# Optimization experiments

Hardware: AMD Instinct MI355X
Metric: run time of the kernel (lower is better)

The kernel has to match this reference:

```python
import jax, jax.numpy as jnp
import numpy as np

C = 19
IGNORE = 255
UPPER_BOUND = 1.0
SEG_W, EDGE_W, ATT_W = 1.0, 0.3, 0.1
EDGE_THRESH = 0.8


def _img_hist(t):
    # torch.histc(target, bins=C, min=0, max=C): bin i counts values in [i, i+1); 255 falls outside
    tf = t.ravel()
    inb = (tf >= 0) & (tf < C)
    idx = jnp.where(inb, tf, 0)
    return jnp.zeros((C,), jnp.float32).at[idx].add(inb.astype(jnp.float32))


def _seg_loss(segin, target):
    # per-image class-histogram weights (ImageBasedCrossEntropyLoss2d, norm=False)
    N = target.shape[0]
    bins = jax.vmap(_img_hist)(target)                      # [N, C]
    hist_norm = bins / jnp.sum(bins, axis=1, keepdims=True)
    w = (bins != 0).astype(jnp.float32) * UPPER_BOUND * (1.0 - hist_norm) + 1.0  # [N, C]

    logp = jax.nn.log_softmax(segin, axis=1)                # [N, C, H, W]
    tc = jnp.clip(target, 0, C - 1)
    lp = jnp.take_along_axis(logp, tc[:, None, :, :], axis=1)[:, 0]  # [N, H, W]
    valid = (target != IGNORE).astype(jnp.float32)
    pw = jnp.take_along_axis(w, tc.reshape(N, -1), axis=1).reshape(target.shape) * valid
    # NLLLoss(weight, reduction='mean', ignore_index): weighted mean per image, summed over batch
    num = -jnp.sum(pw * lp, axis=(1, 2))
    den = jnp.sum(pw, axis=(1, 2))
    return jnp.sum(num / den)


def _bce2d(x, t):
    # x: logits [N,1,H,W]; t: float target, 1=pos, 0=neg, >1 ignored (weight 0)
    pos = t == 1.0
    neg = t == 0.0
    pos_num = jnp.sum(pos.astype(jnp.float32))
    neg_num = jnp.sum(neg.astype(jnp.float32))
    sum_num = pos_num + neg_num
    w = jnp.where(pos, neg_num / sum_num, 0.0) + jnp.where(neg, pos_num / sum_num, 0.0)
    # stable BCE-with-logits
    bce = jnp.maximum(x, 0.0) - x * t + jnp.log1p(jnp.exp(-jnp.abs(x)))
    return jnp.mean(w * bce)


def setup_inputs() -> dict:
    key = jax.random.key(0)
    k1, k2, k3, k4 = jax.random.split(key, 4)
    N, H, W = 4, 768, 768
    segin = jax.random.normal(k1, (N, C, H, W), dtype=jnp.float32)
    edgein = jax.random.normal(k2, (N, 1, H, W), dtype=jnp.float32)
    segmask = jax.random.randint(k3, (N, H, W), 0, C, dtype=jnp.int32)
    edgemask = jax.random.randint(k4, (N, 1, H, W), 0, 2, dtype=jnp.int32)
    return {"segin": segin, "edgein": edgein, "segmask": segmask, "edgemask": edgemask}


def reference(segin, edgein, segmask, edgemask):
    seg_loss = SEG_W * _seg_loss(segin, segmask)
    edge_loss = EDGE_W * _bce2d(edgein, edgemask.astype(jnp.float32))
    # edge attention: pixels where max-channel edge logit > 0.8 keep their label, else ignore
    edge_max = jnp.max(edgein, axis=1)                      # [N, H, W]
    att_target = jnp.where(edge_max > EDGE_THRESH, segmask, IGNORE)
    att_loss = ATT_W * _seg_loss(segin, att_target)
    return seg_loss + edge_loss + att_loss
```

## Files before the change

kernel.cpp:

```cpp
#include <hip/hip_runtime.h>
#include <math.h>

#define CNUM 19
#define NB 4
#define HW 589824
#define NPIX 2359296

struct Ws {
  unsigned int hist_seg[NB][CNUM];
  unsigned int hist_att[NB][CNUM];
  unsigned int pos_num;
  unsigned int neg_num;
  float w_seg[NB][CNUM];
  float w_att[NB][CNUM];
  double num_seg[NB];
  double den_seg[NB];
  double num_att[NB];
  double den_att[NB];
  double bce_sum;
};

__global__ void k_init(Ws* ws) {
  unsigned int* p = (unsigned int*)ws;
  const int nwords = (int)(sizeof(Ws) / 4);
  for (int i = threadIdx.x; i < nwords; i += blockDim.x) p[i] = 0u;
}

__global__ __launch_bounds__(256) void k_hist(const int* __restrict__ segmask,
                                              const float* __restrict__ edgein,
                                              const int* __restrict__ edgemask,
                                              Ws* __restrict__ ws) {
  const int n  = blockIdx.y;
  const int bx = blockIdx.x;
  const int tid = threadIdx.x;
  const int base = n * HW + bx * 4096 + tid * 4;

  unsigned int cs[CNUM], ca[CNUM];
  #pragma unroll
  for (int c = 0; c < CNUM; ++c) { cs[c] = 0u; ca[c] = 0u; }
  unsigned int cp = 0u, cn = 0u;

  #pragma unroll
  for (int it = 0; it < 4; ++it) {
    const int idx = base + it * 1024;
    int4   sv = *reinterpret_cast<const int4*>(segmask + idx);
    float4 e  = *reinterpret_cast<const float4*>(edgein + idx);
    int4   mv = *reinterpret_cast<const int4*>(edgemask + idx);
    int   sa[4] = {sv.x, sv.y, sv.z, sv.w};
    float ea[4] = {e.x, e.y, e.z, e.w};
    int   ma[4] = {mv.x, mv.y, mv.z, mv.w};
    #pragma unroll
    for (int p = 0; p < 4; ++p) {
      const int s = sa[p];
      const bool inb = ((unsigned)s) < (unsigned)CNUM;
      const bool att = inb && (ea[p] > 0.8f);
      #pragma unroll
      for (int c = 0; c < CNUM; ++c) {
        cs[c] += (unsigned)__popcll(__ballot(inb && (s == c)));
        ca[c] += (unsigned)__popcll(__ballot(att && (s == c)));
      }
      cp += (unsigned)__popcll(__ballot(ma[p] == 1));
      cn += (unsigned)__popcll(__ballot(ma[p] == 0));
    }
  }

  __shared__ unsigned int red[4][2 * CNUM + 2];
  const int wave = tid >> 6;
  const int lane = tid & 63;
  if (lane == 0) {
    #pragma unroll
    for (int c = 0; c < CNUM; ++c) { red[wave][c] = cs[c]; red[wave][CNUM + c] = ca[c]; }
    red[wave][2 * CNUM] = cp;
    red[wave][2 * CNUM + 1] = cn;
  }
  __syncthreads();
  if (tid < 2 * CNUM + 2) {
    unsigned int v = red[0][tid] + red[1][tid] + red[2][tid] + red[3][tid];
    if (tid < CNUM)               atomicAdd(&ws->hist_seg[n][tid], v);
    else if (tid < 2 * CNUM)      atomicAdd(&ws->hist_att[n][tid - CNUM], v);
    else if (tid == 2 * CNUM)     atomicAdd(&ws->pos_num, v);
    else                          atomicAdd(&ws->neg_num, v);
  }
}

__global__ void k_weights(Ws* ws) {
  int t = threadIdx.x;
  if (t < 2 * NB * CNUM) {
    int which = t / (NB * CNUM);
    int r = t % (NB * CNUM);
    int n = r / CNUM, c = r % CNUM;
    const unsigned int* h = which ? ws->hist_att[n] : ws->hist_seg[n];
    float total = 0.f;
    #pragma unroll
    for (int i = 0; i < CNUM; ++i) total += (float)h[i];
    float bins = (float)h[c];
    float w = (bins != 0.f ? (1.0f - bins / total) : 0.f) + 1.0f;
    if (which) ws->w_att[n][c] = w;
    else       ws->w_seg[n][c] = w;
  }
}

__global__ __launch_bounds__(256) void k_main(const float* __restrict__ segin,
                                              const float* __restrict__ edgein,
                                              const int* __restrict__ segmask,
                                              const int* __restrict__ edgemask,
                                              const Ws* __restrict__ ws,
                                              Ws* __restrict__ wsw) {
  const int n = blockIdx.y;
  const int tid = threadIdx.x;
  const int hw4 = (blockIdx.x * 256 + tid) * 4;
  const int idx4 = n * HW + hw4;
  const float* base = segin + (size_t)n * CNUM * HW + hw4;

  __shared__ float lws[CNUM], lwa[CNUM];
  if (tid < CNUM) lws[tid] = ws->w_seg[n][tid];
  else if (tid >= 64 && tid < 64 + CNUM) lwa[tid - 64] = ws->w_att[n][tid - 64];
  __syncthreads();

  int4   tm = *reinterpret_cast<const int4*>(segmask + idx4);
  float4 ev = *reinterpret_cast<const float4*>(edgein + idx4);
  int4   em = *reinterpret_cast<const int4*>(edgemask + idx4);
  int   tarr[4]  = {tm.x, tm.y, tm.z, tm.w};
  float earr[4]  = {ev.x, ev.y, ev.z, ev.w};
  int   emarr[4] = {em.x, em.y, em.z, em.w};

  int tc[4];
  #pragma unroll
  for (int p = 0; p < 4; ++p) tc[p] = min(max(tarr[p], 0), CNUM - 1);

  float s[4]  = {0.f, 0.f, 0.f, 0.f};
  float xt[4] = {0.f, 0.f, 0.f, 0.f};
  #pragma unroll
  for (int c = 0; c < CNUM; ++c) {
    float4 v = *reinterpret_cast<const float4*>(base + (size_t)c * HW);
    float va[4] = {v.x, v.y, v.z, v.w};
    #pragma unroll
    for (int p = 0; p < 4; ++p) {
      s[p] += __expf(va[p]);
      xt[p] = (tc[p] == c) ? va[p] : xt[p];
    }
  }

  const unsigned int pn = ws->pos_num, nn = ws->neg_num;
  const float inv_sum = 1.0f / (float)(pn + nn);
  const float wpos = (float)nn * inv_sum;
  const float wneg = (float)pn * inv_sum;

  float acc_num_s = 0.f, acc_den_s = 0.f, acc_num_a = 0.f, acc_den_a = 0.f, acc_bce = 0.f;
  #pragma unroll
  for (int p = 0; p < 4; ++p) {
    float lp = xt[p] - __logf(s[p]);
    bool validt = (tarr[p] != 255);
    float pw_s = validt ? lws[tc[p]] : 0.f;
    acc_num_s -= pw_s * lp;
    acc_den_s += pw_s;

    float e = earr[p];
    bool valida = validt && (e > 0.8f);
    float pw_a = valida ? lwa[tc[p]] : 0.f;
    acc_num_a -= pw_a * lp;
    acc_den_a += pw_a;

    int emv = emarr[p];
    float tf = (float)emv;
    float wb = (emv == 1) ? wpos : ((emv == 0) ? wneg : 0.f);
    float bce = fmaxf(e, 0.f) - e * tf + log1pf(__expf(-fabsf(e)));
    acc_bce += wb * bce;
  }

  #pragma unroll
  for (int off = 32; off > 0; off >>= 1) {
    acc_num_s += __shfl_down(acc_num_s, off);
    acc_den_s += __shfl_down(acc_den_s, off);
    acc_num_a += __shfl_down(acc_num_a, off);
    acc_den_a += __shfl_down(acc_den_a, off);
    acc_bce   += __shfl_down(acc_bce, off);
  }
  __shared__ float red[4][5];
  const int wave = tid >> 6;
  const int lane = tid & 63;
  if (lane == 0) {
    red[wave][0] = acc_num_s; red[wave][1] = acc_den_s;
    red[wave][2] = acc_num_a; red[wave][3] = acc_den_a;
    red[wave][4] = acc_bce;
  }
  __syncthreads();
  if (tid == 0) {
    float r0 = 0.f, r1 = 0.f, r2 = 0.f, r3 = 0.f, r4 = 0.f;
    #pragma unroll
    for (int wv = 0; wv < 4; ++wv) {
      r0 += red[wv][0]; r1 += red[wv][1]; r2 += red[wv][2];
      r3 += red[wv][3]; r4 += red[wv][4];
    }
    atomicAdd(&wsw->num_seg[n], (double)r0);
    atomicAdd(&wsw->den_seg[n], (double)r1);
    atomicAdd(&wsw->num_att[n], (double)r2);
    atomicAdd(&wsw->den_att[n], (double)r3);
    atomicAdd(&wsw->bce_sum,    (double)r4);
  }
}

__global__ void k_final(const Ws* __restrict__ ws, float* __restrict__ out) {
  if (threadIdx.x == 0 && blockIdx.x == 0) {
    double segl = 0.0, attl = 0.0;
    for (int i = 0; i < NB; ++i) {
      segl += ws->num_seg[i] / ws->den_seg[i];
      attl += ws->num_att[i] / ws->den_att[i];
    }
    double edgel = ws->bce_sum / (double)NPIX;
    out[0] = (float)(1.0 * segl + 0.3 * edgel + 0.1 * attl);
  }
}

extern "C" void kernel_launch(void* const* d_in, const int* in_sizes, int n_in,
                              void* d_out, int out_size, void* d_ws, size_t ws_size,
                              hipStream_t stream) {
  const float* segin   = (const float*)d_in[0];
  const float* edgein  = (const float*)d_in[1];
  const int*   segmask = (const int*)d_in[2];
  const int*   edgemask= (const int*)d_in[3];
  Ws* ws = (Ws*)d_ws;
  float* out = (float*)d_out;

  hipLaunchKernelGGL(k_init,    dim3(1),              dim3(256), 0, stream, ws);
  hipLaunchKernelGGL(k_hist,    dim3(HW / 4096, NB),  dim3(256), 0, stream, segmask, edgein, edgemask, ws);
  hipLaunchKernelGGL(k_weights, dim3(1),              dim3(256), 0, stream, ws);
  hipLaunchKernelGGL(k_main,    dim3(HW / 1024, NB),  dim3(256), 0, stream, segin, edgein, segmask, edgemask, ws, ws);
  hipLaunchKernelGGL(k_final,   dim3(1),              dim3(1),   0, stream, ws, out);
}
```

Measured before the change: 355.8 us.

## Fuse weight computation into main kernel and batch-load all channel logits

Removes the separate weights kernel: each main-kernel block now recomputes the per-image class weights from the histograms in shared memory. The main kernel issues all 19 channel float4 loads up front, before the barrier, to expose more memory-level parallelism, and sets launch bounds to cap register use. The histogram kernel reuses a single class ballot ANDed with an attention-mask ballot instead of issuing a second ballot per class. Holding 76 floats per thread raises register pressure, which the occupancy hint may turn into spills.

```diff
diff --git a/kernel.cpp b/kernel.cpp
--- a/kernel.cpp
+++ b/kernel.cpp
@@ -11,8 +11,6 @@
   unsigned int hist_att[NB][CNUM];
   unsigned int pos_num;
   unsigned int neg_num;
-  float w_seg[NB][CNUM];
-  float w_att[NB][CNUM];
   double num_seg[NB];
   double den_seg[NB];
   double num_att[NB];
@@ -53,11 +51,12 @@
     for (int p = 0; p < 4; ++p) {
       const int s = sa[p];
       const bool inb = ((unsigned)s) < (unsigned)CNUM;
-      const bool att = inb && (ea[p] > 0.8f);
+      const unsigned long long attm = __ballot(ea[p] > 0.8f);
       #pragma unroll
       for (int c = 0; c < CNUM; ++c) {
-        cs[c] += (unsigned)__popcll(__ballot(inb && (s == c)));
-        ca[c] += (unsigned)__popcll(__ballot(att && (s == c)));
+        unsigned long long bm = __ballot(inb && (s == c));
+        cs[c] += (unsigned)__popcll(bm);
+        ca[c] += (unsigned)__popcll(bm & attm);
       }
       cp += (unsigned)__popcll(__ballot(ma[p] == 1));
       cn += (unsigned)__popcll(__ballot(ma[p] == 0));
@@ -83,29 +82,12 @@
   }
 }
 
-__global__ void k_weights(Ws* ws) {
-  int t = threadIdx.x;
-  if (t < 2 * NB * CNUM) {
-    int which = t / (NB * CNUM);
-    int r = t % (NB * CNUM);
-    int n = r / CNUM, c = r % CNUM;
-    const unsigned int* h = which ? ws->hist_att[n] : ws->hist_seg[n];
-    float total = 0.f;
-    #pragma unroll
-    for (int i = 0; i < CNUM; ++i) total += (float)h[i];
-    float bins = (float)h[c];
-    float w = (bins != 0.f ? (1.0f - bins / total) : 0.f) + 1.0f;
-    if (which) ws->w_att[n][c] = w;
-    else       ws->w_seg[n][c] = w;
-  }
-}
-
-__global__ __launch_bounds__(256) void k_main(const float* __restrict__ segin,
-                                              const float* __restrict__ edgein,
-                                              const int* __restrict__ segmask,
-                                              const int* __restrict__ edgemask,
-                                              const Ws* __restrict__ ws,
-                                              Ws* __restrict__ wsw) {
+__global__ __launch_bounds__(256, 4) void k_main(const float* __restrict__ segin,
+                                                 const float* __restrict__ edgein,
+                                                 const int* __restrict__ segmask,
+                                                 const int* __restrict__ edgemask,
+                                                 const Ws* __restrict__ ws,
+                                                 Ws* __restrict__ wsw) {
   const int n = blockIdx.y;
   const int tid = threadIdx.x;
   const int hw4 = (blockIdx.x * 256 + tid) * 4;
@@ -113,51 +95,63 @@
   const float* base = segin + (size_t)n * CNUM * HW + hw4;
 
   __shared__ float lws[CNUM], lwa[CNUM];
-  if (tid < CNUM) lws[tid] = ws->w_seg[n][tid];
-  else if (tid >= 64 && tid < 64 + CNUM) lwa[tid - 64] = ws->w_att[n][tid - 64];
-  __syncthreads();
-
+  if (tid < CNUM) {
+    float total = 0.f;
+    #pragma unroll
+    for (int i = 0; i < CNUM; ++i) total += (float)ws->hist_seg[n][i];
+    float bins = (float)ws->hist_seg[n][tid];
+    lws[tid] = (bins != 0.f ? (1.0f - bins / total) : 0.f) + 1.0f;
+  } else if (tid >= 64 && tid < 64 + CNUM) {
+    int c = tid - 64;
+    float total = 0.f;
+    #pragma unroll
+    for (int i = 0; i < CNUM; ++i) total += (float)ws->hist_att[n][i];
+    float bins = (float)ws->hist_att[n][c];
+    lwa[c] = (bins != 0.f ? (1.0f - bins / total) : 0.f) + 1.0f;
+  }
+
+  float4 xv[CNUM];
+  #pragma unroll
+  for (int c = 0; c < CNUM; ++c)
+    xv[c] = *reinterpret_cast<const float4*>(base + (size_t)c * HW);
   int4   tm = *reinterpret_cast<const int4*>(segmask + idx4);
   float4 ev = *reinterpret_cast<const float4*>(edgein + idx4);
   int4   em = *reinterpret_cast<const int4*>(edgemask + idx4);
-  int   tarr[4]  = {tm.x, tm.y, tm.z, tm.w};
-  float earr[4]  = {ev.x, ev.y, ev.z, ev.w};
-  int   emarr[4] = {em.x, em.y, em.z, em.w};
-
-  int tc[4];
-  #pragma unroll
-  for (int p = 0; p < 4; ++p) tc[p] = min(max(tarr[p], 0), CNUM - 1);
-
-  float s[4]  = {0.f, 0.f, 0.f, 0.f};
-  float xt[4] = {0.f, 0.f, 0.f, 0.f};
-  #pragma unroll
-  for (int c = 0; c < CNUM; ++c) {
-    float4 v = *reinterpret_cast<const float4*>(base + (size_t)c * HW);
-    float va[4] = {v.x, v.y, v.z, v.w};
-    #pragma unroll
-    for (int p = 0; p < 4; ++p) {
-      s[p] += __expf(va[p]);
-      xt[p] = (tc[p] == c) ? va[p] : xt[p];
-    }
-  }
 
   const unsigned int pn = ws->pos_num, nn = ws->neg_num;
   const float inv_sum = 1.0f / (float)(pn + nn);
   const float wpos = (float)nn * inv_sum;
   const float wneg = (float)pn * inv_sum;
 
+  __syncthreads();
+
+  int   tarr[4]  = {tm.x, tm.y, tm.z, tm.w};
+  float earr[4]  = {ev.x, ev.y, ev.z, ev.w};
+  int   emarr[4] = {em.x, em.y, em.z, em.w};
+
   float acc_num_s = 0.f, acc_den_s = 0.f, acc_num_a = 0.f, acc_den_a = 0.f, acc_bce = 0.f;
   #pragma unroll
   for (int p = 0; p < 4; ++p) {
-    float lp = xt[p] - __logf(s[p]);
-    bool validt = (tarr[p] != 255);
-    float pw_s = validt ? lws[tc[p]] : 0.f;
+    const int t = tarr[p];
+    const int tc = min(max(t, 0), CNUM - 1);
+    const float* xp = (const float*)&xv[0] + p;
+    float s = 0.f, xt = 0.f;
+    #pragma unroll
+    for (int c = 0; c < CNUM; ++c) {
+      float v = xp[4 * c];
+      s += __expf(v);
+      xt = (tc == c) ? v : xt;
+    }
+    float lp = xt - __logf(s);
+
+    bool validt = (t != 255);
+    float pw_s = validt ? lws[tc] : 0.f;
     acc_num_s -= pw_s * lp;
     acc_den_s += pw_s;
 
     float e = earr[p];
     bool valida = validt && (e > 0.8f);
-    float pw_a = valida ? lwa[tc[p]] : 0.f;
+    float pw_a = valida ? lwa[tc] : 0.f;
     acc_num_a -= pw_a * lp;
     acc_den_a += pw_a;
 
@@ -222,9 +216,8 @@
   Ws* ws = (Ws*)d_ws;
   float* out = (float*)d_out;
 
-  hipLaunchKernelGGL(k_init,    dim3(1),              dim3(256), 0, stream, ws);
-  hipLaunchKernelGGL(k_hist,    dim3(HW / 4096, NB),  dim3(256), 0, stream, segmask, edgein, edgemask, ws);
-  hipLaunchKernelGGL(k_weights, dim3(1),              dim3(256), 0, stream, ws);
-  hipLaunchKernelGGL(k_main,    dim3(HW / 1024, NB),  dim3(256), 0, stream, segin, edgein, segmask, edgemask, ws, ws);
-  hipLaunchKernelGGL(k_final,   dim3(1),              dim3(1),   0, stream, ws, out);
-}
+  hipLaunchKernelGGL(k_init,  dim3(1),             dim3(256), 0, stream, ws);
+  hipLaunchKernelGGL(k_hist,  dim3(HW / 4096, NB), dim3(256), 0, stream, segmask, edgein, edgemask, ws);
+  hipLaunchKernelGGL(k_main,  dim3(HW / 1024, NB), dim3(256), 0, stream, segin, edgein, segmask, edgemask, ws, ws);
+  hipLaunchKernelGGL(k_final, dim3(1),             dim3(1),   0, stream, ws, out);
+}
```

Measured after the change: 345.8 us. 1.03x faster.

## Fold class weights algebraically to single-pass kernel with per-class partial sums

Applied to the files above, without the earlier changes.

Removes the separate histogram and weight kernels by accumulating, per image and class, the count and the sum of -log p. The final kernel then applies the histogram weights algebraically, and does the same for BCE by splitting positive and negative sums. The main kernel also stages segin tiles into LDS through global_load_lds and accumulates per-class sums with shared-memory atomics. This drops a full pass over the masks and two launches, at the cost of contended LDS float atomics and a large LDS footprint that lowers occupancy.

```diff
diff --git a/kernel.cpp b/kernel.cpp
--- a/kernel.cpp
+++ b/kernel.cpp
@@ -5,125 +5,63 @@
 #define NB 4
 #define HW 589824
 #define NPIX 2359296
+#define TILE 1024
 
 struct Ws {
-  unsigned int hist_seg[NB][CNUM];
-  unsigned int hist_att[NB][CNUM];
+  float S_seg[NB][CNUM];
+  float C_seg[NB][CNUM];
+  float S_att[NB][CNUM];
+  float C_att[NB][CNUM];
+  float B_pos;
+  float B_neg;
   unsigned int pos_num;
   unsigned int neg_num;
-  float w_seg[NB][CNUM];
-  float w_att[NB][CNUM];
-  double num_seg[NB];
-  double den_seg[NB];
-  double num_att[NB];
-  double den_att[NB];
-  double bce_sum;
 };
 
 __global__ void k_init(Ws* ws) {
   unsigned int* p = (unsigned int*)ws;
-  const int nwords = (int)(sizeof(Ws) / 4);
-  for (int i = threadIdx.x; i < nwords; i += blockDim.x) p[i] = 0u;
+  const int nw = (int)(sizeof(Ws) / 4);
+  for (int i = threadIdx.x; i < nw; i += blockDim.x) p[i] = 0u;
 }
 
-__global__ __launch_bounds__(256) void k_hist(const int* __restrict__ segmask,
-                                              const float* __restrict__ edgein,
-                                              const int* __restrict__ edgemask,
-                                              Ws* __restrict__ ws) {
-  const int n  = blockIdx.y;
-  const int bx = blockIdx.x;
+__global__ __launch_bounds__(256, 2) void k_main(const float* __restrict__ segin,
+                                                 const float* __restrict__ edgein,
+                                                 const int* __restrict__ segmask,
+                                                 const int* __restrict__ edgemask,
+                                                 Ws* __restrict__ ws) {
+  const int n = blockIdx.y;
   const int tid = threadIdx.x;
-  const int base = n * HW + bx * 4096 + tid * 4;
+  const int wave = tid >> 6;
+  const int lane = tid & 63;
+  const int tile0 = blockIdx.x * TILE;
 
-  unsigned int cs[CNUM], ca[CNUM];
-  #pragma unroll
-  for (int c = 0; c < CNUM; ++c) { cs[c] = 0u; ca[c] = 0u; }
-  unsigned int cp = 0u, cn = 0u;
+  __shared__ float xs[CNUM][TILE];
+  __shared__ float aSs[CNUM], aCs[CNUM], aSa[CNUM], aCa[CNUM];
+  __shared__ float redf[4][2];
+  __shared__ unsigned int redu[4][2];
 
-  #pragma unroll
-  for (int it = 0; it < 4; ++it) {
-    const int idx = base + it * 1024;
-    int4   sv = *reinterpret_cast<const int4*>(segmask + idx);
-    float4 e  = *reinterpret_cast<const float4*>(edgein + idx);
-    int4   mv = *reinterpret_cast<const int4*>(edgemask + idx);
-    int   sa[4] = {sv.x, sv.y, sv.z, sv.w};
-    float ea[4] = {e.x, e.y, e.z, e.w};
-    int   ma[4] = {mv.x, mv.y, mv.z, mv.w};
+  if (tid < CNUM) { aSs[tid] = 0.f; aCs[tid] = 0.f; aSa[tid] = 0.f; aCa[tid] = 0.f; }
+
+  {
+    const float* g0 = segin + (size_t)n * CNUM * HW + tile0 + wave * 256 + lane * 4;
     #pragma unroll
-    for (int p = 0; p < 4; ++p) {
-      const int s = sa[p];
-      const bool inb = ((unsigned)s) < (unsigned)CNUM;
-      const bool att = inb && (ea[p] > 0.8f);
-      #pragma unroll
-      for (int c = 0; c < CNUM; ++c) {
-        cs[c] += (unsigned)__popcll(__ballot(inb && (s == c)));
-        ca[c] += (unsigned)__popcll(__ballot(att && (s == c)));
-      }
-      cp += (unsigned)__popcll(__ballot(ma[p] == 1));
-      cn += (unsigned)__popcll(__ballot(ma[p] == 0));
+    for (int c = 0; c < CNUM; ++c) {
+      __builtin_amdgcn_global_load_lds(
+          (const __attribute__((address_space(1))) void*)(g0 + (size_t)c * HW),
+          (__attribute__((address_space(3))) void*)(&xs[c][wave * 256]),
+          16, 0, 0);
     }
   }
+  const int px = n * HW + tile0 + tid * 4;
+  int4   tm = *reinterpret_cast<const int4*>(segmask + px);
+  float4 ev = *reinterpret_cast<const float4*>(edgein + px);
+  int4   em = *reinterpret_cast<const int4*>(edgemask + px);
 
-  __shared__ unsigned int red[4][2 * CNUM + 2];
-  const int wave = tid >> 6;
-  const int lane = tid & 63;
-  if (lane == 0) {
-    #pragma unroll
-    for (int c = 0; c < CNUM; ++c) { red[wave][c] = cs[c]; red[wave][CNUM + c] = ca[c]; }
-    red[wave][2 * CNUM] = cp;
-    red[wave][2 * CNUM + 1] = cn;
-  }
-  __syncthreads();
-  if (tid < 2 * CNUM + 2) {
-    unsigned int v = red[0][tid] + red[1][tid] + red[2][tid] + red[3][tid];
-    if (tid < CNUM)               atomicAdd(&ws->hist_seg[n][tid], v);
-    else if (tid < 2 * CNUM)      atomicAdd(&ws->hist_att[n][tid - CNUM], v);
-    else if (tid == 2 * CNUM)     atomicAdd(&ws->pos_num, v);
-    else                          atomicAdd(&ws->neg_num, v);
-  }
-}
-
-__global__ void k_weights(Ws* ws) {
-  int t = threadIdx.x;
-  if (t < 2 * NB * CNUM) {
-    int which = t / (NB * CNUM);
-    int r = t % (NB * CNUM);
-    int n = r / CNUM, c = r % CNUM;
-    const unsigned int* h = which ? ws->hist_att[n] : ws->hist_seg[n];
-    float total = 0.f;
-    #pragma unroll
-    for (int i = 0; i < CNUM; ++i) total += (float)h[i];
-    float bins = (float)h[c];
-    float w = (bins != 0.f ? (1.0f - bins / total) : 0.f) + 1.0f;
-    if (which) ws->w_att[n][c] = w;
-    else       ws->w_seg[n][c] = w;
-  }
-}
-
-__global__ __launch_bounds__(256) void k_main(const float* __restrict__ segin,
-                                              const float* __restrict__ edgein,
-                                              const int* __restrict__ segmask,
-                                              const int* __restrict__ edgemask,
-                                              const Ws* __restrict__ ws,
-                                              Ws* __restrict__ wsw) {
-  const int n = blockIdx.y;
-  const int tid = threadIdx.x;
-  const int hw4 = (blockIdx.x * 256 + tid) * 4;
-  const int idx4 = n * HW + hw4;
-  const float* base = segin + (size_t)n * CNUM * HW + hw4;
-
-  __shared__ float lws[CNUM], lwa[CNUM];
-  if (tid < CNUM) lws[tid] = ws->w_seg[n][tid];
-  else if (tid >= 64 && tid < 64 + CNUM) lwa[tid - 64] = ws->w_att[n][tid - 64];
   __syncthreads();
 
-  int4   tm = *reinterpret_cast<const int4*>(segmask + idx4);
-  float4 ev = *reinterpret_cast<const float4*>(edgein + idx4);
-  int4   em = *reinterpret_cast<const int4*>(edgemask + idx4);
   int   tarr[4]  = {tm.x, tm.y, tm.z, tm.w};
   float earr[4]  = {ev.x, ev.y, ev.z, ev.w};
   int   emarr[4] = {em.x, em.y, em.z, em.w};
-
   int tc[4];
   #pragma unroll
   for (int p = 0; p < 4; ++p) tc[p] = min(max(tarr[p], 0), CNUM - 1);
@@ -132,7 +70,7 @@
   float xt[4] = {0.f, 0.f, 0.f, 0.f};
   #pragma unroll
   for (int c = 0; c < CNUM; ++c) {
-    float4 v = *reinterpret_cast<const float4*>(base + (size_t)c * HW);
+    float4 v = *reinterpret_cast<const float4*>(&xs[c][tid * 4]);
     float va[4] = {v.x, v.y, v.z, v.w};
     #pragma unroll
     for (int p = 0; p < 4; ++p) {
@@ -141,74 +79,84 @@
     }
   }
 
-  const unsigned int pn = ws->pos_num, nn = ws->neg_num;
-  const float inv_sum = 1.0f / (float)(pn + nn);
-  const float wpos = (float)nn * inv_sum;
-  const float wneg = (float)pn * inv_sum;
-
-  float acc_num_s = 0.f, acc_den_s = 0.f, acc_num_a = 0.f, acc_den_a = 0.f, acc_bce = 0.f;
+  float bp = 0.f, bn = 0.f;
+  unsigned int cp = 0u, cn = 0u;
   #pragma unroll
   for (int p = 0; p < 4; ++p) {
     float lp = xt[p] - __logf(s[p]);
-    bool validt = (tarr[p] != 255);
-    float pw_s = validt ? lws[tc[p]] : 0.f;
-    acc_num_s -= pw_s * lp;
-    acc_den_s += pw_s;
-
+    bool valid = (tarr[p] != 255);
+    if (valid) {
+      atomicAdd(&aSs[tc[p]], -lp);
+      atomicAdd(&aCs[tc[p]], 1.f);
+      if (earr[p] > 0.8f) {
+        atomicAdd(&aSa[tc[p]], -lp);
+        atomicAdd(&aCa[tc[p]], 1.f);
+      }
+    }
     float e = earr[p];
-    bool valida = validt && (e > 0.8f);
-    float pw_a = valida ? lwa[tc[p]] : 0.f;
-    acc_num_a -= pw_a * lp;
-    acc_den_a += pw_a;
-
     int emv = emarr[p];
-    float tf = (float)emv;
-    float wb = (emv == 1) ? wpos : ((emv == 0) ? wneg : 0.f);
-    float bce = fmaxf(e, 0.f) - e * tf + log1pf(__expf(-fabsf(e)));
-    acc_bce += wb * bce;
+    float bce = fmaxf(e, 0.f) - e * (float)emv + log1pf(__expf(-fabsf(e)));
+    bp += (emv == 1) ? bce : 0.f;
+    bn += (emv == 0) ? bce : 0.f;
+    cp += (emv == 1) ? 1u : 0u;
+    cn += (emv == 0) ? 1u : 0u;
   }
 
   #pragma unroll
   for (int off = 32; off > 0; off >>= 1) {
-    acc_num_s += __shfl_down(acc_num_s, off);
-    acc_den_s += __shfl_down(acc_den_s, off);
-    acc_num_a += __shfl_down(acc_num_a, off);
-    acc_den_a += __shfl_down(acc_den_a, off);
-    acc_bce   += __shfl_down(acc_bce, off);
+    bp += __shfl_down(bp, off);
+    bn += __shfl_down(bn, off);
+    cp += __shfl_down(cp, off);
+    cn += __shfl_down(cn, off);
   }
-  __shared__ float red[4][5];
-  const int wave = tid >> 6;
-  const int lane = tid & 63;
-  if (lane == 0) {
-    red[wave][0] = acc_num_s; red[wave][1] = acc_den_s;
-    red[wave][2] = acc_num_a; red[wave][3] = acc_den_a;
-    red[wave][4] = acc_bce;
-  }
+  if (lane == 0) { redf[wave][0] = bp; redf[wave][1] = bn;
+                   redu[wave][0] = cp; redu[wave][1] = cn; }
   __syncthreads();
   if (tid == 0) {
-    float r0 = 0.f, r1 = 0.f, r2 = 0.f, r3 = 0.f, r4 = 0.f;
-    #pragma unroll
-    for (int wv = 0; wv < 4; ++wv) {
-      r0 += red[wv][0]; r1 += red[wv][1]; r2 += red[wv][2];
-      r3 += red[wv][3]; r4 += red[wv][4];
-    }
-    atomicAdd(&wsw->num_seg[n], (double)r0);
-    atomicAdd(&wsw->den_seg[n], (double)r1);
-    atomicAdd(&wsw->num_att[n], (double)r2);
-    atomicAdd(&wsw->den_att[n], (double)r3);
-    atomicAdd(&wsw->bce_sum,    (double)r4);
+    float tbp = redf[0][0] + redf[1][0] + redf[2][0] + redf[3][0];
+    float tbn = redf[0][1] + redf[1][1] + redf[2][1] + redf[3][1];
+    unsigned int tcp = redu[0][0] + redu[1][0] + redu[2][0] + redu[3][0];
+    unsigned int tcn = redu[0][1] + redu[1][1] + redu[2][1] + redu[3][1];
+    atomicAdd(&ws->B_pos, tbp);
+    atomicAdd(&ws->B_neg, tbn);
+    atomicAdd(&ws->pos_num, tcp);
+    atomicAdd(&ws->neg_num, tcn);
+  }
+  if (tid < CNUM) {
+    atomicAdd(&ws->S_seg[n][tid], aSs[tid]);
+    atomicAdd(&ws->C_seg[n][tid], aCs[tid]);
+    atomicAdd(&ws->S_att[n][tid], aSa[tid]);
+    atomicAdd(&ws->C_att[n][tid], aCa[tid]);
   }
 }
 
 __global__ void k_final(const Ws* __restrict__ ws, float* __restrict__ out) {
   if (threadIdx.x == 0 && blockIdx.x == 0) {
     double segl = 0.0, attl = 0.0;
-    for (int i = 0; i < NB; ++i) {
-      segl += ws->num_seg[i] / ws->den_seg[i];
-      attl += ws->num_att[i] / ws->den_att[i];
+    for (int n = 0; n < NB; ++n) {
+      double tot = 0.0, num = 0.0, den = 0.0;
+      for (int c = 0; c < CNUM; ++c) tot += (double)ws->C_seg[n][c];
+      for (int c = 0; c < CNUM; ++c) {
+        double b = (double)ws->C_seg[n][c];
+        double w = (b != 0.0 ? (1.0 - b / tot) : 0.0) + 1.0;
+        num += w * (double)ws->S_seg[n][c];
+        den += w * b;
+      }
+      segl += num / den;
+      double tota = 0.0, numa = 0.0, dena = 0.0;
+      for (int c = 0; c < CNUM; ++c) tota += (double)ws->C_att[n][c];
+      for (int c = 0; c < CNUM; ++c) {
+        double b = (double)ws->C_att[n][c];
+        double w = (b != 0.0 ? (1.0 - b / tota) : 0.0) + 1.0;
+        numa += w * (double)ws->S_att[n][c];
+        dena += w * b;
+      }
+      attl += numa / dena;
     }
-    double edgel = ws->bce_sum / (double)NPIX;
-    out[0] = (float)(1.0 * segl + 0.3 * edgel + 0.1 * attl);
+    double pos = (double)ws->pos_num, neg = (double)ws->neg_num;
+    double wpos = neg / (pos + neg), wneg = pos / (pos + neg);
+    double edgel = (wpos * (double)ws->B_pos + wneg * (double)ws->B_neg) / (double)NPIX;
+    out[0] = (float)(segl + 0.3 * edgel + 0.1 * attl);
   }
 }
 
@@ -222,9 +170,8 @@
   Ws* ws = (Ws*)d_ws;
   float* out = (float*)d_out;
 
-  hipLaunchKernelGGL(k_init,    dim3(1),              dim3(256), 0, stream, ws);
-  hipLaunchKernelGGL(k_hist,    dim3(HW / 4096, NB),  dim3(256), 0, stream, segmask, edgein, edgemask, ws);
-  hipLaunchKernelGGL(k_weights, dim3(1),              dim3(256), 0, stream, ws);
-  hipLaunchKernelGGL(k_main,    dim3(HW / 1024, NB),  dim3(256), 0, stream, segin, edgein, segmask, edgemask, ws, ws);
-  hipLaunchKernelGGL(k_final,   dim3(1),              dim3(1),   0, stream, ws, out);
+  hipLaunchKernelGGL(k_init,  dim3(1),              dim3(128), 0, stream, ws);
+  hipLaunchKernelGGL(k_main,  dim3(HW / TILE, NB),  dim3(256), 0, stream,
+                     segin, edgein, segmask, edgemask, ws);
+  hipLaunchKernelGGL(k_final, dim3(1),              dim3(1),   0, stream, ws, out);
 }
```

Result: no change. 359.1 us (+0.9%).
